# Optimization experiments

Measured on AMD Instinct MI355X. Metric: run time of the kernel, lower is better.

## Reference

```python
import jax, jax.numpy as jnp
import numpy as np

N_NODES = 50000
N_EDGES = 800000
D = 128
HEADS = 4
HEAD_DIM = D // HEADS
N_LAYERS = 3
NEG_SLOPE = 0.2


def setup_inputs() -> dict:
    key = jax.random.key(0)
    ks = jax.random.split(key, 10)
    x = jax.random.normal(ks[0], (N_NODES, D), dtype=jnp.float32)
    edge_index = jax.random.randint(ks[1], (2, N_EDGES), 0, N_NODES, dtype=jnp.int32)
    s = 1.0 / np.sqrt(D)
    gcn_w = jax.random.normal(ks[2], (N_LAYERS, D, D), dtype=jnp.float32) * s
    gcn_b = jnp.zeros((N_LAYERS, D), dtype=jnp.float32)
    gat_w = jax.random.normal(ks[3], (N_LAYERS, D, D), dtype=jnp.float32) * s
    gat_att_src = jax.random.normal(ks[4], (N_LAYERS, HEADS, HEAD_DIM), dtype=jnp.float32) * s
    gat_att_dst = jax.random.normal(ks[5], (N_LAYERS, HEADS, HEAD_DIM), dtype=jnp.float32) * s
    gat_b = jnp.zeros((N_LAYERS, D), dtype=jnp.float32)
    ln_g = jnp.ones((N_LAYERS, D), dtype=jnp.float32)
    ln_b = jnp.zeros((N_LAYERS, D), dtype=jnp.float32)
    return {"x": x, "edge_index": edge_index, "gcn_w": gcn_w, "gcn_b": gcn_b,
            "gat_w": gat_w, "gat_att_src": gat_att_src, "gat_att_dst": gat_att_dst,
            "gat_b": gat_b, "ln_g": ln_g, "ln_b": ln_b}


def _gcn(x, src, dst, n, w, b):
    # PyG GCNConv: self-loops (already in src/dst), symmetric normalization
    xw = x @ w                                             # [N, D]
    deg = jax.ops.segment_sum(jnp.ones_like(dst, dtype=xw.dtype), dst, num_segments=n)
    dinv = jax.lax.rsqrt(deg)                              # deg >= 1 due to self-loops
    norm = dinv[src] * dinv[dst]                           # [E]
    out = jax.ops.segment_sum(xw[src] * norm[:, None], dst, num_segments=n)
    return out + b


def _gat(x, src, dst, n, w, att_src, att_dst, b):
    # PyG GATConv, concat heads, self-loops already in src/dst
    xw = (x @ w).reshape(n, HEADS, HEAD_DIM)               # [N, H, Dh]
    a_src = (xw * att_src).sum(-1)                         # [N, H]
    a_dst = (xw * att_dst).sum(-1)                         # [N, H]
    e = jax.nn.leaky_relu(a_src[src] + a_dst[dst], NEG_SLOPE)  # [E, H]
    m = jax.ops.segment_max(e, dst, num_segments=n)        # [N, H]
    ee = jnp.exp(e - m[dst])
    z = jax.ops.segment_sum(ee, dst, num_segments=n)       # [N, H]
    alpha = ee / z[dst]                                    # [E, H]
    out = jax.ops.segment_sum(xw[src] * alpha[:, :, None], dst, num_segments=n)
    return out.reshape(n, HEADS * HEAD_DIM) + b


def _layernorm(x, g, b, eps=1e-5):
    mu = x.mean(-1, keepdims=True)
    var = ((x - mu) ** 2).mean(-1, keepdims=True)
    return (x - mu) * jax.lax.rsqrt(var + eps) * g + b


def reference(x, edge_index, gcn_w, gcn_b, gat_w, gat_att_src, gat_att_dst, gat_b, ln_g, ln_b):
    n = x.shape[0]
    loops = jnp.arange(n, dtype=edge_index.dtype)
    src = jnp.concatenate([edge_index[0], loops])
    dst = jnp.concatenate([edge_index[1], loops])
    h = x
    for i in range(N_LAYERS):
        h_gcn = _gcn(h, src, dst, n, gcn_w[i], gcn_b[i])
        h_att = _gat(h_gcn, src, dst, n, gat_w[i], gat_att_src[i], gat_att_dst[i], gat_b[i])
        h = _layernorm(h_att + h_gcn, ln_g[i], ln_b[i])
        h = jax.nn.relu(h)  # dropout is identity in eval mode
    return h
```

## Files before the change

### kernel.cpp

```cpp
#include <hip/hip_runtime.h>

#define NN 50000
#define NE 800000
#define NOUT (NN * 128)
#define PF_TOTAL 100608
#define NCHUNK 8
#define CHUNKSZ 6250
#define NC4 (NN * NCHUNK)

typedef unsigned int u32;
typedef unsigned short u16;

typedef __attribute__((ext_vector_type(4))) float f32x4;
typedef __attribute__((ext_vector_type(8))) short bf16x8;

__device__ __forceinline__ float bf2f(u16 u) { return __uint_as_float(((u32)u) << 16); }
__device__ __forceinline__ u32 f2bf_u(float f) {
  u32 u = __float_as_uint(f);
  u += 0x7FFFu + ((u >> 16) & 1u);
  return u >> 16;
}
__device__ __forceinline__ u32 pk2(float a, float b) {
  return f2bf_u(a) | (f2bf_u(b) << 16);
}
__device__ __forceinline__ float lo_f(u32 v) { return __uint_as_float(v << 16); }
__device__ __forceinline__ float hi_f(u32 v) { return __uint_as_float(v & 0xFFFF0000u); }
__device__ __forceinline__ float h2f(u16 h) {
  u32 sg = ((u32)h >> 15) & 1u, e = ((u32)h >> 10) & 0x1Fu, mm = (u32)h & 0x3FFu;
  u32 o;
  if (e == 0u) o = sg << 31;
  else if (e == 31u) o = (sg << 31) | 0x7F800000u | (mm << 13);
  else o = (sg << 31) | ((e + 112u) << 23) | (mm << 13);
  return __uint_as_float(o);
}
__device__ __forceinline__ float lrelu(float x) { return x > 0.f ? x : 0.2f * x; }
__device__ __forceinline__ u32 umin32(u32 a, u32 b) { return a < b ? a : b; }

__device__ __forceinline__ float cvt_one(const void* p, int j, u32 fmode) {
  if (fmode == 1u) return ((const float*)p)[j];
  if (fmode == 2u) return h2f(((const u16*)p)[j]);
  return bf2f(((const u16*)p)[j]);
}

__global__ __launch_bounds__(256) void MultiScaleGNN_54769422958784_kernel(
    float* out, float val, int n) {
  int i = blockIdx.x * 256 + threadIdx.x;
  if (i < n) out[i] = val;
}

__global__ __launch_bounds__(64) void detect_kernel(const u32* lng, const int* ei,
                                                    u32* flag) {
  if (threadIdx.x == 0) {
    u32 v0 = lng[0], v1 = lng[1];
    u32 fm;
    if (v0 == 0x3F803F80u && v1 == 0x3F803F80u) fm = 0u;
    else if (v0 == 0x3F800000u && v1 == 0x3F800000u) fm = 1u;
    else if (v0 == 0x3C003C00u && v1 == 0x3C003C00u) fm = 2u;
    else fm = 1u;
    flag[0] = fm;
    flag[1] = ((ei[1] | ei[3] | ei[5] | ei[7]) == 0) ? 1u : 0u;
  }
}

__global__ __launch_bounds__(256) void cvt_x_kernel(const void* in, u32* outh, int n64,
                                                    const u32* flag) {
  u32 fm = flag[0];
  int i = blockIdx.x * 256 + threadIdx.x;
  if (i >= n64) return;
  int node = i >> 6, w = i & 63;
  float a = cvt_one(in, node * 128 + w * 2, fm);
  float b = cvt_one(in, node * 128 + w * 2 + 1, fm);
  outh[i] = pk2(a, b);
}

__global__ __launch_bounds__(256) void cvt_params_kernel(const void* g0, const void* g1,
                                                         const void* g2, const void* g3,
                                                         const void* g4, const void* g5,
                                                         const void* g6, const void* g7,
                                                         float* out, const u32* flag) {
  u32 fm = flag[0];
  int i = blockIdx.x * 256 + threadIdx.x;
  if (i >= PF_TOTAL) return;
  int offs[9] = {0, 49152, 49536, 98688, 99072, 99456, 99840, 100224, 100608};
  const void* ptrs[8] = {g0, g1, g2, g3, g4, g5, g6, g7};
  int r = 0;
  while (i >= offs[r + 1]) r++;
  out[i] = cvt_one(ptrs[r], i - offs[r], fm);
}

__global__ __launch_bounds__(256) void cvt_wt_kernel(const float* __restrict__ pf,
                                                     u32* __restrict__ wt) {
  int i = blockIdx.x * 256 + threadIdx.x;
  if (i >= 49152) return;
  int mat = i >> 13;
  int rem = i & 8191;
  int kk = rem >> 7;
  int n = rem & 127;
  const float* W = pf + (mat < 3 ? (size_t)mat * 16384 : 49536 + (size_t)(mat - 3) * 16384);
  float a = W[(2 * kk) * 128 + n];
  float b = W[(2 * kk + 1) * 128 + n];
  wt[(size_t)mat * 8192 + n * 64 + kk] = pk2(a, b);
}

__global__ __launch_bounds__(256) void zero1_kernel(u32* a, int n) {
  int i = blockIdx.x * 256 + threadIdx.x;
  if (i < n) a[i] = 0u;
}

__global__ __launch_bounds__(256) void rank_kernel(const int* ei, u32* cnt, u32* rank,
                                                   int e, int n, const u32* flag) {
  int i = blockIdx.x * blockDim.x + threadIdx.x;
  if (i >= e) return;
  u32 em = flag[1];
  int s = em ? ei[2 * i] : ei[i];
  int d = em ? ei[2 * e + 2 * i] : ei[e + i];
  int sp = ((u32)s < (u32)n) ? s : 0;
  u32 r = 0u;
  if ((u32)d < (u32)n) r = atomicAdd(&cnt[d * NCHUNK + sp / CHUNKSZ], 1u);
  rank[i] = r;
}

__device__ __forceinline__ u32 wave_incl_scan(u32 v, int lane) {
#pragma unroll
  for (int off = 1; off < 64; off <<= 1) {
    u32 t = (u32)__shfl_up((int)v, off);
    if (lane >= off) v += t;
  }
  return v;
}

__global__ __launch_bounds__(256) void scan_sum_kernel(const u32* counts, u32* bsums,
                                                       int n) {
  __shared__ u32 ws[4];
  int tid = threadIdx.x, lane = tid & 63, wid = tid >> 6;
  int i0 = blockIdx.x * 1024 + tid * 4;
  u32 t = 0u;
#pragma unroll
  for (int k = 0; k < 4; k++) t += (i0 + k < n) ? counts[i0 + k] : 0u;
#pragma unroll
  for (int off = 32; off; off >>= 1) t += (u32)__shfl_xor((int)t, off);
  if (lane == 0) ws[wid] = t;
  __syncthreads();
  if (tid == 0) bsums[blockIdx.x] = ws[0] + ws[1] + ws[2] + ws[3];
}

__global__ __launch_bounds__(512) void scan_bsums_kernel(u32* bsums, u32* rowptr, int nb,
                                                         int n) {
  __shared__ u32 ws[8];
  int tid = threadIdx.x, lane = tid & 63, wid = tid >> 6;
  u32 v = (tid < nb) ? bsums[tid] : 0u;
  u32 incl = wave_incl_scan(v, lane);
  if (lane == 63) ws[wid] = incl;
  __syncthreads();
  u32 wo = 0u;
  for (int w = 0; w < wid; w++) wo += ws[w];
  u32 excl = incl - v + wo;
  if (tid < nb) bsums[tid] = excl;
  if (tid == 0) {
    u32 tot = 0u;
    for (int w = 0; w < 8; w++) tot += ws[w];
    rowptr[n] = tot;
  }
}

__global__ __launch_bounds__(256) void scan_write_kernel(const u32* counts,
                                                         const u32* bsums, u32* rowptr,
                                                         int n) {
  __shared__ u32 ws[4];
  int tid = threadIdx.x, lane = tid & 63, wid = tid >> 6;
  int b = blockIdx.x;
  int i0 = b * 1024 + tid * 4;
  u32 c0 = (i0 + 0 < n) ? counts[i0 + 0] : 0u;
  u32 c1 = (i0 + 1 < n) ? counts[i0 + 1] : 0u;
  u32 c2 = (i0 + 2 < n) ? counts[i0 + 2] : 0u;
  u32 c3 = (i0 + 3 < n) ? counts[i0 + 3] : 0u;
  u32 ts = c0 + c1 + c2 + c3;
  u32 incl = wave_incl_scan(ts, lane);
  if (lane == 63) ws[wid] = incl;
  __syncthreads();
  u32 wo = bsums[b];
  for (int w = 0; w < wid; w++) wo += ws[w];
  u32 excl = incl - ts + wo;
  if (i0 + 0 < n) rowptr[i0 + 0] = excl;
  excl += c0;
  if (i0 + 1 < n) rowptr[i0 + 1] = excl;
  excl += c1;
  if (i0 + 2 < n) rowptr[i0 + 2] = excl;
  excl += c2;
  if (i0 + 3 < n) rowptr[i0 + 3] = excl;
}

__global__ __launch_bounds__(256) void dinv_kernel(const u32* __restrict__ rowptr4,
                                                   float* __restrict__ dinv, int nn) {
  int i = blockIdx.x * 256 + threadIdx.x;
  if (i < nn)
    dinv[i] = rsqrtf((float)(rowptr4[(size_t)i * NCHUNK + NCHUNK] -
                             rowptr4[(size_t)i * NCHUNK] + 1u));
}

__global__ __launch_bounds__(256) void place_kernel(const int* ei, const u32* rowptr4,
                                                    const u32* rank, int* col, int e,
                                                    int n, const u32* flag) {
  int i = blockIdx.x * blockDim.x + threadIdx.x;
  if (i >= e) return;
  u32 em = flag[1];
  int s = em ? ei[2 * i] : ei[i];
  int d = em ? ei[2 * e + 2 * i] : ei[e + i];
  if ((u32)d >= (u32)n) return;
  int sp = ((u32)s < (u32)n) ? s : 0;
  u32 p = rowptr4[(size_t)d * NCHUNK + sp / CHUNKSZ] + rank[i];
  if (p < (u32)e) col[p] = sp;
}

__global__ __launch_bounds__(256) void gemm_mfma_kernel(
    const u32* __restrict__ Ah, const u32* __restrict__ WTh, u32* __restrict__ Oh,
    const float* __restrict__ dinv, const float* __restrict__ att_s,
    const float* __restrict__ att_d, float* __restrict__ asrc,
    float* __restrict__ adst, int M) {
  int tid = threadIdx.x;
  int wave = tid >> 6, lane = tid & 63;
  int p = lane & 15, g = lane >> 4;
  int r0 = blockIdx.x * 128 + wave * 32;
  int ra = r0 + p, rb = r0 + 16 + p;
  int rac = min(ra, M - 1), rbc = min(rb, M - 1);

  const u32* apA = Ah + (size_t)rac * 64 + g * 4;
  const u32* apB = Ah + (size_t)rbc * 64 + g * 4;
  uint4 bA[4], bB[4];
#pragma unroll
  for (int k0 = 0; k0 < 4; k0++) {
    bA[k0] = *(const uint4*)(apA + k0 * 16);
    bB[k0] = *(const uint4*)(apB + k0 * 16);
  }

  f32x4 acc0[8], acc1[8];
#pragma unroll
  for (int t = 0; t < 8; t++) {
    acc0[t] = (f32x4)0.f;
    acc1[t] = (f32x4)0.f;
  }

  const u32* wp = WTh + p * 64 + g * 4;
#pragma unroll
  for (int k0 = 0; k0 < 4; k0++) {
    bf16x8 fa = __builtin_bit_cast(bf16x8, bA[k0]);
    bf16x8 fb = __builtin_bit_cast(bf16x8, bB[k0]);
#pragma unroll
    for (int t = 0; t < 8; t++) {
      uint4 af = *(const uint4*)(wp + t * 1024 + k0 * 16);
      bf16x8 aw = __builtin_bit_cast(bf16x8, af);
      acc0[t] = __builtin_amdgcn_mfma_f32_16x16x32_bf16(aw, fa, acc0[t], 0, 0, 0);
      acc1[t] = __builtin_amdgcn_mfma_f32_16x16x32_bf16(aw, fb, acc1[t], 0, 0, 0);
    }
  }

#pragma unroll
  for (int i = 0; i < 2; i++) {
    int r = r0 + i * 16 + p;
    if (r < M) {
      float sc = dinv ? dinv[r] : 1.0f;
      u32* orow = Oh + (size_t)r * 64;
      float hs[4] = {0.f, 0.f, 0.f, 0.f};
      float hd[4] = {0.f, 0.f, 0.f, 0.f};
#pragma unroll
      for (int t = 0; t < 8; t++) {
        f32x4 v = (i == 0) ? acc0[t] : acc1[t];
        float v0 = v[0] * sc, v1 = v[1] * sc, v2 = v[2] * sc, v3 = v[3] * sc;
        *(uint2*)(orow + t * 8 + g * 2) = make_uint2(pk2(v0, v1), pk2(v2, v3));
        if (att_s) {
          float4 wsv = *(const float4*)(att_s + t * 16 + g * 4);
          float4 wdv = *(const float4*)(att_d + t * 16 + g * 4);
          int h = t >> 1;
          hs[h] += v0 * wsv.x + v1 * wsv.y + v2 * wsv.z + v3 * wsv.w;
          hd[h] += v0 * wdv.x + v1 * wdv.y + v2 * wdv.z + v3 * wdv.w;
        }
      }
      if (att_s) {
#pragma unroll
        for (int h = 0; h < 4; h++) {
          hs[h] += __shfl_xor(hs[h], 16);
          hs[h] += __shfl_xor(hs[h], 32);
          hd[h] += __shfl_xor(hd[h], 16);
          hd[h] += __shfl_xor(hd[h], 32);
        }
        if (g == 0) {
          *(float4*)(asrc + (size_t)r * 4) = make_float4(hs[0], hs[1], hs[2], hs[3]);
          *(float4*)(adst + (size_t)r * 4) = make_float4(hd[0], hd[1], hd[2], hd[3]);
        }
      }
    }
  }
}

__global__ __launch_bounds__(256) void gcn_agg_kernel(const u32* __restrict__ xh,
                                                      const int* col, const u32* rowptr4,
                                                      const float* dinv, const float* bias,
                                                      u32* __restrict__ outh, int n) {
  __shared__ int lds_s[8][32];
  int g = threadIdx.x >> 5;
  int l = threadIdx.x & 31;
  int d = blockIdx.x * 8 + g;
  if (d >= n) return;
  u32 start = umin32(rowptr4[(size_t)d * NCHUNK], (u32)NE);
  u32 end = umin32(rowptr4[(size_t)d * NCHUNK + NCHUNK], (u32)NE);
  float4 acc = make_float4(0.f, 0.f, 0.f, 0.f);
  for (u32 base = start; base < end; base += 32) {
    u32 i = base + l;
    int cnt = (int)umin32(32u, end - base);
    if (i < end) lds_s[g][l] = col[i];
#pragma unroll 4
    for (int j = 0; j < cnt; j++) {
      int s = lds_s[g][j];
      uint2 v = *(const uint2*)(xh + (size_t)s * 64 + l * 2);
      acc.x += lo_f(v.x);
      acc.y += hi_f(v.x);
      acc.z += lo_f(v.y);
      acc.w += hi_f(v.y);
    }
  }
  int c0 = l * 4;
  uint2 sv = *(const uint2*)(xh + (size_t)d * 64 + l * 2);
  float dd = dinv[d];
  float o0 = dd * (acc.x + lo_f(sv.x)) + bias[c0];
  float o1 = dd * (acc.y + hi_f(sv.x)) + bias[c0 + 1];
  float o2 = dd * (acc.z + lo_f(sv.y)) + bias[c0 + 2];
  float o3 = dd * (acc.w + hi_f(sv.y)) + bias[c0 + 3];
  *(uint2*)(outh + (size_t)d * 64 + l * 2) = make_uint2(pk2(o0, o1), pk2(o2, o3));
}

__global__ __launch_bounds__(256) void gat_agg_kernel(
    const u32* __restrict__ xh, const float* a_src4, const float* a_dst4, const int* col,
    const u32* rowptr4, const u32* __restrict__ hgcnh, const float* gat_b,
    const float* ln_g, const float* ln_b, u32* __restrict__ outh,
    float* __restrict__ outf, int n) {
  __shared__ u32 lds_s[8][32];
  __shared__ float lds_ee[8][32][4];
  int g = threadIdx.x >> 5;
  int l = threadIdx.x & 31;
  int head4 = l >> 3;
  int d = blockIdx.x * 8 + g;
  if (d >= n) return;
  u32 start = umin32(rowptr4[(size_t)d * NCHUNK], (u32)NE);
  u32 end = umin32(rowptr4[(size_t)d * NCHUNK + NCHUNK], (u32)NE);
  float4 ad = *(const float4*)(a_dst4 + (size_t)d * 4);
  float4 asl = *(const float4*)(a_src4 + (size_t)d * 4);
  float4 es;
  es.x = lrelu(asl.x + ad.x);
  es.y = lrelu(asl.y + ad.y);
  es.z = lrelu(asl.z + ad.z);
  es.w = lrelu(asl.w + ad.w);
  float4 m = es;
  float4 zp = make_float4(0.f, 0.f, 0.f, 0.f);
  float4 acc = make_float4(0.f, 0.f, 0.f, 0.f);
  for (u32 base = start; base < end; base += 32) {
    u32 i = base + l;
    int cnt = (int)umin32(32u, end - base);
    bool act = i < end;
    float4 lg = make_float4(-1e30f, -1e30f, -1e30f, -1e30f);
    int s = 0;
    if (act) {
      s = col[i];
      float4 a = *(const float4*)(a_src4 + (size_t)s * 4);
      lg.x = lrelu(a.x + ad.x);
      lg.y = lrelu(a.y + ad.y);
      lg.z = lrelu(a.z + ad.z);
      lg.w = lrelu(a.w + ad.w);
    }
    float4 cm = lg;
#pragma unroll
    for (int off = 16; off; off >>= 1) {
      cm.x = fmaxf(cm.x, __shfl_xor(cm.x, off));
      cm.y = fmaxf(cm.y, __shfl_xor(cm.y, off));
      cm.z = fmaxf(cm.z, __shfl_xor(cm.z, off));
      cm.w = fmaxf(cm.w, __shfl_xor(cm.w, off));
    }
    float4 mn;
    mn.x = fmaxf(m.x, cm.x);
    mn.y = fmaxf(m.y, cm.y);
    mn.z = fmaxf(m.z, cm.z);
    mn.w = fmaxf(m.w, cm.w);
    float4 f;
    f.x = __expf(m.x - mn.x);
    f.y = __expf(m.y - mn.y);
    f.z = __expf(m.z - mn.z);
    f.w = __expf(m.w - mn.w);
    m = mn;
    zp.x *= f.x;
    zp.y *= f.y;
    zp.z *= f.z;
    zp.w *= f.w;
    float fsel = (head4 == 0) ? f.x : (head4 == 1) ? f.y : (head4 == 2) ? f.z : f.w;
    acc.x *= fsel;
    acc.y *= fsel;
    acc.z *= fsel;
    acc.w *= fsel;
    if (act) {
      float ex = __expf(lg.x - m.x);
      float ey = __expf(lg.y - m.y);
      float ez = __expf(lg.z - m.z);
      float ew = __expf(lg.w - m.w);
      zp.x += ex;
      zp.y += ey;
      zp.z += ez;
      zp.w += ew;
      lds_s[g][l] = (u32)s;
      *(float4*)&lds_ee[g][l][0] = make_float4(ex, ey, ez, ew);
    }
#pragma unroll 4
    for (int j = 0; j < cnt; j++) {
      u32 sg = lds_s[g][j];
      float w = lds_ee[g][j][head4];
      uint2 v = *(const uint2*)(xh + (size_t)sg * 64 + l * 2);
      acc.x = fmaf(w, lo_f(v.x), acc.x);
      acc.y = fmaf(w, hi_f(v.x), acc.y);
      acc.z = fmaf(w, lo_f(v.y), acc.z);
      acc.w = fmaf(w, hi_f(v.y), acc.w);
    }
  }
  float4 ees;
  ees.x = __expf(es.x - m.x);
  ees.y = __expf(es.y - m.y);
  ees.z = __expf(es.z - m.z);
  ees.w = __expf(es.w - m.w);
#pragma unroll
  for (int off = 16; off; off >>= 1) {
    zp.x += __shfl_xor(zp.x, off);
    zp.y += __shfl_xor(zp.y, off);
    zp.z += __shfl_xor(zp.z, off);
    zp.w += __shfl_xor(zp.w, off);
  }
  zp.x += ees.x;
  zp.y += ees.y;
  zp.z += ees.z;
  zp.w += ees.w;
  float wsel = (head4 == 0) ? ees.x : (head4 == 1) ? ees.y : (head4 == 2) ? ees.z : ees.w;
  float zsel = (head4 == 0) ? zp.x : (head4 == 1) ? zp.y : (head4 == 2) ? zp.z : zp.w;
  int c0 = l * 4;
  uint2 sv = *(const uint2*)(xh + (size_t)d * 64 + l * 2);
  acc.x = fmaf(wsel, lo_f(sv.x), acc.x);
  acc.y = fmaf(wsel, hi_f(sv.x), acc.y);
  acc.z = fmaf(wsel, lo_f(sv.y), acc.z);
  acc.w = fmaf(wsel, hi_f(sv.y), acc.w);
  float rz = 1.0f / zsel;
  uint2 hgv = *(const uint2*)(hgcnh + (size_t)d * 64 + l * 2);
  float t0 = acc.x * rz + gat_b[c0] + lo_f(hgv.x);
  float t1 = acc.y * rz + gat_b[c0 + 1] + hi_f(hgv.x);
  float t2 = acc.z * rz + gat_b[c0 + 2] + lo_f(hgv.y);
  float t3 = acc.w * rz + gat_b[c0 + 3] + hi_f(hgv.y);
  float ssum = t0 + t1 + t2 + t3;
#pragma unroll
  for (int off = 16; off; off >>= 1) ssum += __shfl_xor(ssum, off);
  float mu = ssum * (1.0f / 128.0f);
  float d0 = t0 - mu, d1 = t1 - mu, d2 = t2 - mu, d3 = t3 - mu;
  float vv = d0 * d0 + d1 * d1 + d2 * d2 + d3 * d3;
#pragma unroll
  for (int off = 16; off; off >>= 1) vv += __shfl_xor(vv, off);
  float rstd = rsqrtf(vv * (1.0f / 128.0f) + 1e-5f);
  float o0 = fmaxf(fmaf(d0 * rstd, ln_g[c0], ln_b[c0]), 0.f);
  float o1 = fmaxf(fmaf(d1 * rstd, ln_g[c0 + 1], ln_b[c0 + 1]), 0.f);
  float o2 = fmaxf(fmaf(d2 * rstd, ln_g[c0 + 2], ln_b[c0 + 2]), 0.f);
  float o3 = fmaxf(fmaf(d3 * rstd, ln_g[c0 + 3], ln_b[c0 + 3]), 0.f);
  if (outf) {
    *(float4*)(outf + (size_t)d * 128 + c0) = make_float4(o0, o1, o2, o3);
  } else {
    *(uint2*)(outh + (size_t)d * 64 + l * 2) = make_uint2(pk2(o0, o1), pk2(o2, o3));
  }
}

extern "C" void kernel_launch(void* const* d_in, const int* in_sizes, int n_in,
                              void* d_out, int out_size, void* d_ws, size_t ws_size,
                              hipStream_t stream) {
  const int N = NN, E = NE;
  (void)in_sizes;
  (void)n_in;
  (void)out_size;
  (void)ws_size;

  char* ws = (char*)d_ws;
  size_t off = 0;
  u32* xwh = (u32*)(ws + off);      off += (size_t)N * 64 * 4;
  u32* hbufh = (u32*)(ws + off);    off += (size_t)N * 64 * 4;
  u32* hgcnh = (u32*)(ws + off);    off += (size_t)N * 64 * 4;
  float* asrc = (float*)(ws + off); off += (size_t)N * 4 * 4;
  float* adst = (float*)(ws + off); off += (size_t)N * 4 * 4;
  float* dinv = (float*)(ws + off); off += (size_t)N * 4;
  u32* counts4 = (u32*)(ws + off);  off += (size_t)NC4 * 4;
  u32* rowptr4 = (u32*)(ws + off);  off += (size_t)(NC4 + 1) * 4 + 252;
  u32* rank = (u32*)(ws + off);     off += (size_t)E * 4;
  int* col = (int*)(ws + off);      off += (size_t)E * 4;
  float* pf = (float*)(ws + off);   off += (size_t)PF_TOTAL * 4;
  u32* wt = (u32*)(ws + off);       off += (size_t)49152 * 4;
  u32* bsums = (u32*)(ws + off);    off += 512 * 4;
  u32* flag = (u32*)(ws + off);     off += 256;

  const int* edge_index = (const int*)d_in[1];
  detect_kernel<<<1, 64, 0, stream>>>((const u32*)d_in[8], edge_index, flag);
  cvt_params_kernel<<<(PF_TOTAL + 255) / 256, 256, 0, stream>>>(
      d_in[2], d_in[3], d_in[4], d_in[5], d_in[6], d_in[7], d_in[8], d_in[9], pf, flag);
  cvt_wt_kernel<<<(49152 + 255) / 256, 256, 0, stream>>>(pf, wt);
  cvt_x_kernel<<<(N * 64 + 255) / 256, 256, 0, stream>>>(d_in[0], hbufh, N * 64, flag);
  zero1_kernel<<<(NC4 + 255) / 256, 256, 0, stream>>>(counts4, NC4);
  rank_kernel<<<(E + 255) / 256, 256, 0, stream>>>(edge_index, counts4, rank, E, N, flag);
  {
    int nb = (NC4 + 1023) / 1024;
    scan_sum_kernel<<<nb, 256, 0, stream>>>(counts4, bsums, NC4);
    scan_bsums_kernel<<<1, 512, 0, stream>>>(bsums, rowptr4, nb, NC4);
    scan_write_kernel<<<nb, 256, 0, stream>>>(counts4, bsums, rowptr4, NC4);
  }
  dinv_kernel<<<(N + 255) / 256, 256, 0, stream>>>(rowptr4, dinv, N);
  place_kernel<<<(E + 255) / 256, 256, 0, stream>>>(edge_index, rowptr4, rank, col, E, N,
                                                    flag);

  const float* att_s = pf + 98688;
  const float* att_d = pf + 99072;
  const float* gcn_b = pf + 49152;
  const float* gat_b = pf + 99456;
  const float* ln_g = pf + 99840;
  const float* ln_b = pf + 100224;

  int gblocks = (N + 127) / 128;
  int ablocks = (N + 7) / 8;
  for (int l = 0; l < 3; l++) {
    gemm_mfma_kernel<<<gblocks, 256, 0, stream>>>(
        hbufh, wt + (size_t)l * 8192, xwh, dinv, (const float*)0, (const float*)0,
        (float*)0, (float*)0, N);
    gcn_agg_kernel<<<ablocks, 256, 0, stream>>>(xwh, col, rowptr4, dinv, gcn_b + l * 128,
                                                hgcnh, N);
    gemm_mfma_kernel<<<gblocks, 256, 0, stream>>>(
        hgcnh, wt + (size_t)(3 + l) * 8192, xwh, (const float*)0, att_s + l * 128,
        att_d + l * 128, asrc, adst, N);
    gat_agg_kernel<<<ablocks, 256, 0, stream>>>(
        xwh, asrc, adst, col, rowptr4, hgcnh, gat_b + l * 128, ln_g + l * 128,
        ln_b + l * 128, hbufh, (l < 2) ? (float*)0 : (float*)d_out, N);
  }
}
```

Before: 479.0 us.

## Fold self-loops into CSR, drop source chunking, use MFMA for GCN aggregation

Self-loop edges are now added to the CSR build itself, so GAT no longer special-cases the self term and the degree is read straight from rowptr. The per-destination source-chunk bucketing (8 chunks per node) is removed, which shrinks the count/scan arrays eightfold but loses source-sorted locality within each row. GCN aggregation is rewritten as a wave-level MFMA: 16 destinations share one gathered edge tile staged in LDS, and a 0/1 selector matrix does the segment sum. The MFMA path wastes compute on padding and adds LDS traffic in place of plain scalar accumulation.

```diff
diff --git a/kernel.cpp b/kernel.cpp
--- a/kernel.cpp
+++ b/kernel.cpp
@@ -2,11 +2,9 @@
 
 #define NN 50000
 #define NE 800000
+#define NE2 (NE + NN)
 #define NOUT (NN * 128)
 #define PF_TOTAL 100608
-#define NCHUNK 8
-#define CHUNKSZ 6250
-#define NC4 (NN * NCHUNK)
 
 typedef unsigned int u32;
 typedef unsigned short u16;
@@ -110,13 +108,18 @@
 __global__ __launch_bounds__(256) void rank_kernel(const int* ei, u32* cnt, u32* rank,
                                                    int e, int n, const u32* flag) {
   int i = blockIdx.x * blockDim.x + threadIdx.x;
-  if (i >= e) return;
-  u32 em = flag[1];
-  int s = em ? ei[2 * i] : ei[i];
-  int d = em ? ei[2 * e + 2 * i] : ei[e + i];
-  int sp = ((u32)s < (u32)n) ? s : 0;
+  if (i >= e + n) return;
+  int s, d;
+  if (i < e) {
+    u32 em = flag[1];
+    s = em ? ei[2 * i] : ei[i];
+    d = em ? ei[2 * e + 2 * i] : ei[e + i];
+  } else {
+    s = d = i - e;
+  }
+  (void)s;
   u32 r = 0u;
-  if ((u32)d < (u32)n) r = atomicAdd(&cnt[d * NCHUNK + sp / CHUNKSZ], 1u);
+  if ((u32)d < (u32)n) r = atomicAdd(&cnt[d], 1u);
   rank[i] = r;
 }
 
@@ -190,26 +193,29 @@
   if (i0 + 3 < n) rowptr[i0 + 3] = excl;
 }
 
-__global__ __launch_bounds__(256) void dinv_kernel(const u32* __restrict__ rowptr4,
+__global__ __launch_bounds__(256) void dinv_kernel(const u32* __restrict__ rowptr,
                                                    float* __restrict__ dinv, int nn) {
   int i = blockIdx.x * 256 + threadIdx.x;
-  if (i < nn)
-    dinv[i] = rsqrtf((float)(rowptr4[(size_t)i * NCHUNK + NCHUNK] -
-                             rowptr4[(size_t)i * NCHUNK] + 1u));
-}
-
-__global__ __launch_bounds__(256) void place_kernel(const int* ei, const u32* rowptr4,
+  if (i < nn) dinv[i] = rsqrtf((float)(rowptr[i + 1] - rowptr[i]));
+}
+
+__global__ __launch_bounds__(256) void place_kernel(const int* ei, const u32* rowptr,
                                                     const u32* rank, int* col, int e,
                                                     int n, const u32* flag) {
   int i = blockIdx.x * blockDim.x + threadIdx.x;
-  if (i >= e) return;
-  u32 em = flag[1];
-  int s = em ? ei[2 * i] : ei[i];
-  int d = em ? ei[2 * e + 2 * i] : ei[e + i];
+  if (i >= e + n) return;
+  int s, d;
+  if (i < e) {
+    u32 em = flag[1];
+    s = em ? ei[2 * i] : ei[i];
+    d = em ? ei[2 * e + 2 * i] : ei[e + i];
+  } else {
+    s = d = i - e;
+  }
   if ((u32)d >= (u32)n) return;
   int sp = ((u32)s < (u32)n) ? s : 0;
-  u32 p = rowptr4[(size_t)d * NCHUNK + sp / CHUNKSZ] + rank[i];
-  if (p < (u32)e) col[p] = sp;
+  u32 p = rowptr[d] + rank[i];
+  if (p < (u32)NE2) col[p] = sp;
 }
 
 __global__ __launch_bounds__(256) void gemm_mfma_kernel(
@@ -292,45 +298,86 @@
   }
 }
 
-__global__ __launch_bounds__(256) void gcn_agg_kernel(const u32* __restrict__ xh,
-                                                      const int* col, const u32* rowptr4,
-                                                      const float* dinv, const float* bias,
-                                                      u32* __restrict__ outh, int n) {
-  __shared__ int lds_s[8][32];
-  int g = threadIdx.x >> 5;
-  int l = threadIdx.x & 31;
-  int d = blockIdx.x * 8 + g;
-  if (d >= n) return;
-  u32 start = umin32(rowptr4[(size_t)d * NCHUNK], (u32)NE);
-  u32 end = umin32(rowptr4[(size_t)d * NCHUNK + NCHUNK], (u32)NE);
-  float4 acc = make_float4(0.f, 0.f, 0.f, 0.f);
+__global__ __launch_bounds__(256) void gcn_spmm_kernel(
+    const u32* __restrict__ xh, const int* __restrict__ col,
+    const u32* __restrict__ rowptr, const float* __restrict__ dinv,
+    const float* __restrict__ bias, u32* __restrict__ outh, int n) {
+  __shared__ u32 XT[4][64][36];
+  int wv = threadIdx.x >> 6, lane = threadIdx.x & 63;
+  int p = lane & 15, g = lane >> 4;
+  int d0 = (blockIdx.x * 4 + wv) * 16;
+  int dp = min(d0 + p, n);
+  u32 rp = rowptr[dp];
+  u32 rpn = rowptr[min(dp + 1, n)];
+  u32 start = (u32)__shfl((int)rp, 0);
+  u32 end = (u32)__shfl((int)rpn, 15);
+  f32x4 acc[8];
+#pragma unroll
+  for (int t = 0; t < 8; t++) acc[t] = (f32x4)0.f;
+
   for (u32 base = start; base < end; base += 32) {
-    u32 i = base + l;
     int cnt = (int)umin32(32u, end - base);
-    if (i < end) lds_s[g][l] = col[i];
-#pragma unroll 4
-    for (int j = 0; j < cnt; j++) {
-      int s = lds_s[g][j];
-      uint2 v = *(const uint2*)(xh + (size_t)s * 64 + l * 2);
-      acc.x += lo_f(v.x);
-      acc.y += hi_f(v.x);
-      acc.z += lo_f(v.y);
-      acc.w += hi_f(v.y);
-    }
-  }
-  int c0 = l * 4;
-  uint2 sv = *(const uint2*)(xh + (size_t)d * 64 + l * 2);
-  float dd = dinv[d];
-  float o0 = dd * (acc.x + lo_f(sv.x)) + bias[c0];
-  float o1 = dd * (acc.y + hi_f(sv.x)) + bias[c0 + 1];
-  float o2 = dd * (acc.z + lo_f(sv.y)) + bias[c0 + 2];
-  float o3 = dd * (acc.w + hi_f(sv.y)) + bias[c0 + 3];
-  *(uint2*)(outh + (size_t)d * 64 + l * 2) = make_uint2(pk2(o0, o1), pk2(o2, o3));
+    int colreg = 0;
+    if (lane < cnt) colreg = col[base + lane];
+#pragma unroll 8
+    for (int r = 0; r < 32; r++) {
+      int s = __shfl(colreg, r);
+      u32 q = 0u;
+      if (r < cnt) q = xh[(size_t)s * 64 + lane];
+      XT[wv][lane][r] = q;
+    }
+    u32 pf[4];
+#pragma unroll
+    for (int jj = 0; jj < 4; jj++) {
+      u32 e0 = base + (u32)(g * 8 + jj * 2);
+      u32 e1 = e0 + 1u;
+      u32 lo = (e0 >= rp && e0 < rpn) ? 0x3F80u : 0u;
+      u32 hi = (e1 >= rp && e1 < rpn) ? 0x3F80u : 0u;
+      pf[jj] = lo | (hi << 16);
+    }
+    bf16x8 pa = __builtin_bit_cast(bf16x8, make_uint4(pf[0], pf[1], pf[2], pf[3]));
+#pragma unroll
+    for (int t = 0; t < 8; t++) {
+      int ch = t * 16 + p;
+      int cp = ch >> 1, half = ch & 1;
+      const u32* xr = &XT[wv][cp][g * 8];
+      uint4 qa = *(const uint4*)(xr);
+      uint4 qb = *(const uint4*)(xr + 4);
+      u32 b0, b1, b2, b3;
+      if (half) {
+        b0 = (qa.x >> 16) | (qa.y & 0xFFFF0000u);
+        b1 = (qa.z >> 16) | (qa.w & 0xFFFF0000u);
+        b2 = (qb.x >> 16) | (qb.y & 0xFFFF0000u);
+        b3 = (qb.z >> 16) | (qb.w & 0xFFFF0000u);
+      } else {
+        b0 = (qa.x & 0xFFFFu) | (qa.y << 16);
+        b1 = (qa.z & 0xFFFFu) | (qa.w << 16);
+        b2 = (qb.x & 0xFFFFu) | (qb.y << 16);
+        b3 = (qb.z & 0xFFFFu) | (qb.w << 16);
+      }
+      bf16x8 bb = __builtin_bit_cast(bf16x8, make_uint4(b0, b1, b2, b3));
+      acc[t] = __builtin_amdgcn_mfma_f32_16x16x32_bf16(pa, bb, acc[t], 0, 0, 0);
+    }
+  }
+
+#pragma unroll
+  for (int t = 0; t < 8; t++) {
+    int ch = t * 16 + p;
+    f32x4 v = acc[t];
+#pragma unroll
+    for (int i = 0; i < 4; i++) {
+      int d = d0 + g * 4 + i;
+      float o = (d < n) ? (v[i] * dinv[d] + bias[ch]) : 0.f;
+      float other = __shfl_xor(o, 1);
+      if ((p & 1) == 0 && d < n)
+        outh[(size_t)d * 64 + (ch >> 1)] = pk2(o, other);
+    }
+  }
 }
 
 __global__ __launch_bounds__(256) void gat_agg_kernel(
     const u32* __restrict__ xh, const float* a_src4, const float* a_dst4, const int* col,
-    const u32* rowptr4, const u32* __restrict__ hgcnh, const float* gat_b,
+    const u32* rowptr, const u32* __restrict__ hgcnh, const float* gat_b,
     const float* ln_g, const float* ln_b, u32* __restrict__ outh,
     float* __restrict__ outf, int n) {
   __shared__ u32 lds_s[8][32];
@@ -340,16 +387,9 @@
   int head4 = l >> 3;
   int d = blockIdx.x * 8 + g;
   if (d >= n) return;
-  u32 start = umin32(rowptr4[(size_t)d * NCHUNK], (u32)NE);
-  u32 end = umin32(rowptr4[(size_t)d * NCHUNK + NCHUNK], (u32)NE);
+  u32 start = umin32(rowptr[d], (u32)NE2), end = umin32(rowptr[d + 1], (u32)NE2);
   float4 ad = *(const float4*)(a_dst4 + (size_t)d * 4);
-  float4 asl = *(const float4*)(a_src4 + (size_t)d * 4);
-  float4 es;
-  es.x = lrelu(asl.x + ad.x);
-  es.y = lrelu(asl.y + ad.y);
-  es.z = lrelu(asl.z + ad.z);
-  es.w = lrelu(asl.w + ad.w);
-  float4 m = es;
+  float4 m = make_float4(-1e30f, -1e30f, -1e30f, -1e30f);
   float4 zp = make_float4(0.f, 0.f, 0.f, 0.f);
   float4 acc = make_float4(0.f, 0.f, 0.f, 0.f);
   for (u32 base = start; base < end; base += 32) {
@@ -417,11 +457,6 @@
       acc.w = fmaf(w, hi_f(v.y), acc.w);
     }
   }
-  float4 ees;
-  ees.x = __expf(es.x - m.x);
-  ees.y = __expf(es.y - m.y);
-  ees.z = __expf(es.z - m.z);
-  ees.w = __expf(es.w - m.w);
 #pragma unroll
   for (int off = 16; off; off >>= 1) {
     zp.x += __shfl_xor(zp.x, off);
@@ -429,18 +464,8 @@
     zp.z += __shfl_xor(zp.z, off);
     zp.w += __shfl_xor(zp.w, off);
   }
-  zp.x += ees.x;
-  zp.y += ees.y;
-  zp.z += ees.z;
-  zp.w += ees.w;
-  float wsel = (head4 == 0) ? ees.x : (head4 == 1) ? ees.y : (head4 == 2) ? ees.z : ees.w;
   float zsel = (head4 == 0) ? zp.x : (head4 == 1) ? zp.y : (head4 == 2) ? zp.z : zp.w;
   int c0 = l * 4;
-  uint2 sv = *(const uint2*)(xh + (size_t)d * 64 + l * 2);
-  acc.x = fmaf(wsel, lo_f(sv.x), acc.x);
-  acc.y = fmaf(wsel, hi_f(sv.x), acc.y);
-  acc.z = fmaf(wsel, lo_f(sv.y), acc.z);
-  acc.w = fmaf(wsel, hi_f(sv.y), acc.w);
   float rz = 1.0f / zsel;
   uint2 hgv = *(const uint2*)(hgcnh + (size_t)d * 64 + l * 2);
   float t0 = acc.x * rz + gat_b[c0] + lo_f(hgv.x);
@@ -484,10 +509,10 @@
   float* asrc = (float*)(ws + off); off += (size_t)N * 4 * 4;
   float* adst = (float*)(ws + off); off += (size_t)N * 4 * 4;
   float* dinv = (float*)(ws + off); off += (size_t)N * 4;
-  u32* counts4 = (u32*)(ws + off);  off += (size_t)NC4 * 4;
-  u32* rowptr4 = (u32*)(ws + off);  off += (size_t)(NC4 + 1) * 4 + 252;
-  u32* rank = (u32*)(ws + off);     off += (size_t)E * 4;
-  int* col = (int*)(ws + off);      off += (size_t)E * 4;
+  u32* counts = (u32*)(ws + off);   off += (size_t)N * 4;
+  u32* rowptr = (u32*)(ws + off);   off += (size_t)(N + 1) * 4 + 252;
+  u32* rank = (u32*)(ws + off);     off += (size_t)NE2 * 4;
+  int* col = (int*)(ws + off);      off += (size_t)NE2 * 4;
   float* pf = (float*)(ws + off);   off += (size_t)PF_TOTAL * 4;
   u32* wt = (u32*)(ws + off);       off += (size_t)49152 * 4;
   u32* bsums = (u32*)(ws + off);    off += 512 * 4;
@@ -499,17 +524,18 @@
       d_in[2], d_in[3], d_in[4], d_in[5], d_in[6], d_in[7], d_in[8], d_in[9], pf, flag);
   cvt_wt_kernel<<<(49152 + 255) / 256, 256, 0, stream>>>(pf, wt);
   cvt_x_kernel<<<(N * 64 + 255) / 256, 256, 0, stream>>>(d_in[0], hbufh, N * 64, flag);
-  zero1_kernel<<<(NC4 + 255) / 256, 256, 0, stream>>>(counts4, NC4);
-  rank_kernel<<<(E + 255) / 256, 256, 0, stream>>>(edge_index, counts4, rank, E, N, flag);
+  zero1_kernel<<<(N + 255) / 256, 256, 0, stream>>>(counts, N);
+  rank_kernel<<<(NE2 + 255) / 256, 256, 0, stream>>>(edge_index, counts, rank, E, N,
+                                                     flag);
   {
-    int nb = (NC4 + 1023) / 1024;
-    scan_sum_kernel<<<nb, 256, 0, stream>>>(counts4, bsums, NC4);
-    scan_bsums_kernel<<<1, 512, 0, stream>>>(bsums, rowptr4, nb, NC4);
-    scan_write_kernel<<<nb, 256, 0, stream>>>(counts4, bsums, rowptr4, NC4);
-  }
-  dinv_kernel<<<(N + 255) / 256, 256, 0, stream>>>(rowptr4, dinv, N);
-  place_kernel<<<(E + 255) / 256, 256, 0, stream>>>(edge_index, rowptr4, rank, col, E, N,
-                                                    flag);
+    int nb = (N + 1023) / 1024;
+    scan_sum_kernel<<<nb, 256, 0, stream>>>(counts, bsums, N);
+    scan_bsums_kernel<<<1, 512, 0, stream>>>(bsums, rowptr, nb, N);
+    scan_write_kernel<<<nb, 256, 0, stream>>>(counts, bsums, rowptr, N);
+  }
+  dinv_kernel<<<(N + 255) / 256, 256, 0, stream>>>(rowptr, dinv, N);
+  place_kernel<<<(NE2 + 255) / 256, 256, 0, stream>>>(edge_index, rowptr, rank, col, E,
+                                                      N, flag);
 
   const float* att_s = pf + 98688;
   const float* att_d = pf + 99072;
@@ -519,18 +545,19 @@
   const float* ln_b = pf + 100224;
 
   int gblocks = (N + 127) / 128;
+  int sblocks = (N + 63) / 64;
   int ablocks = (N + 7) / 8;
   for (int l = 0; l < 3; l++) {
     gemm_mfma_kernel<<<gblocks, 256, 0, stream>>>(
         hbufh, wt + (size_t)l * 8192, xwh, dinv, (const float*)0, (const float*)0,
         (float*)0, (float*)0, N);
-    gcn_agg_kernel<<<ablocks, 256, 0, stream>>>(xwh, col, rowptr4, dinv, gcn_b + l * 128,
-                                                hgcnh, N);
+    gcn_spmm_kernel<<<sblocks, 256, 0, stream>>>(xwh, col, rowptr, dinv,
+                                                 gcn_b + l * 128, hgcnh, N);
     gemm_mfma_kernel<<<gblocks, 256, 0, stream>>>(
         hgcnh, wt + (size_t)(3 + l) * 8192, xwh, (const float*)0, att_s + l * 128,
         att_d + l * 128, asrc, adst, N);
     gat_agg_kernel<<<ablocks, 256, 0, stream>>>(
-        xwh, asrc, adst, col, rowptr4, hgcnh, gat_b + l * 128, ln_g + l * 128,
+        xwh, asrc, adst, col, rowptr, hgcnh, gat_b + l * 128, ln_g + l * 128,
         ln_b + l * 128, hbufh, (l < 2) ? (float*)0 : (float*)d_out, N);
   }
 }
```

After: 726.0 us. +51.6%, slower.
